# Performance work log

Hardware: AMD Instinct MI355X
Metric: run time of the kernel (lower is better)

Reference implementation:

```python
import jax, jax.numpy as jnp
import numpy as np

N = 10000   # nodes
E = 320000  # edges
G = 64      # graphs in batch
D = 256     # gnn embedding dim
A = 118     # atomic_num_dim
OUT = 100   # spectrum dim
NUM_GINE = 2


def setup_inputs() -> dict:
    key = jax.random.key(0)
    ks = jax.random.split(key, 16)
    inp = {
        'atomic_num': jax.random.normal(ks[0], (N, A), dtype=jnp.float32),
        'length': jax.random.uniform(ks[1], (E,), dtype=jnp.float32),
        'src': jax.random.randint(ks[2], (E,), 0, N, dtype=jnp.int32),
        'dst': jax.random.randint(ks[3], (E,), 0, N, dtype=jnp.int32),
        'graph_ids': jnp.sort(jax.random.randint(ks[4], (N,), 0, G, dtype=jnp.int32)),
        # parameters
        'W_node': jax.random.normal(ks[5], (A, D), dtype=jnp.float32) / np.sqrt(A),
        'b_node': jnp.zeros((D,), dtype=jnp.float32),
        'W_edge': jax.random.normal(ks[6], (1, D), dtype=jnp.float32),
        'b_edge': jnp.zeros((D,), dtype=jnp.float32),
        'gine_eps': jnp.zeros((NUM_GINE,), dtype=jnp.float32),  # learnable eps per GINEConv
        'W_gnn': jax.random.normal(ks[7], (NUM_GINE, D, D), dtype=jnp.float32) / np.sqrt(D),
        'b_gnn': jnp.zeros((NUM_GINE, D), dtype=jnp.float32),
        'eps_param': jnp.array([1e-3], dtype=jnp.float32),  # unify_vector eps
        'W_mlp': jax.random.normal(ks[8], (D, OUT), dtype=jnp.float32) / np.sqrt(D),
        'b_mlp': jnp.zeros((OUT,), dtype=jnp.float32),
    }
    return inp


def reference(atomic_num, length, src, dst, graph_ids,
              W_node, b_node, W_edge, b_edge,
              gine_eps, W_gnn, b_gnn, eps_param, W_mlp, b_mlp):
    # node / edge embeddings
    h = atomic_num @ W_node + b_node            # [N, D]
    e = length[:, None] @ W_edge + b_edge       # [E, D]
    # GINEConv layers: m_ij = relu(h_src + e_ij); h_i' = W((1+eps)h_i + sum_j m_ij) + b
    for i in range(NUM_GINE):
        m = jax.nn.relu(h[src] + e)             # [E, D] gather + elementwise
        agg = jax.ops.segment_sum(m, dst, num_segments=N)  # scatter-sum to dst nodes
        h = ((1.0 + gine_eps[i]) * h + agg) @ W_gnn[i] + b_gnn[i]
    # sum_nodes pooling per graph
    feat = jax.ops.segment_sum(h, graph_ids, num_segments=G)  # [G, D]
    # unify_vector: global min/max normalization
    mn = jnp.min(feat)
    mx = jnp.max(feat)
    feat = (feat - mn) / (eps_param[0] + mx - mn)
    # MLP head (no hidden layers): Linear(D, 100)
    return feat @ W_mlp + b_mlp                 # [G, 100]
```

## Files before the change

### kernel.cpp

```cpp
#include <hip/hip_runtime.h>
#include <hip/hip_bf16.h>

#define N_NODES 10000
#define N_EDGES 320000
#define N_GRAPHS 64
#define DIM 256
#define ADIM 118
#define OUTD 100
#define CAP 192

typedef short bf8_t __attribute__((ext_vector_type(8)));
typedef float f4_t  __attribute__((ext_vector_type(4)));

__device__ __forceinline__ unsigned short f2bf(float f) {
    unsigned u = __float_as_uint(f);
    u += 0x7FFFu + ((u >> 16) & 1u);
    return (unsigned short)(u >> 16);
}
__device__ __forceinline__ float bf2f(unsigned short s) {
    return __uint_as_float(((unsigned)s) << 16);
}

__global__ __launch_bounds__(256) void convW_k(
    const float* __restrict__ Wn, const float* __restrict__ Wg,
    unsigned short* __restrict__ WnT, unsigned short* __restrict__ WgT,
    int* __restrict__ cursor, float* __restrict__ feat) {
    int i = blockIdx.x * 256 + threadIdx.x;
    if (i < 32768) {
        int c = i >> 7, k = i & 127;
        WnT[i] = (k < ADIM) ? f2bf(Wn[k * DIM + c]) : (unsigned short)0;
    } else {
        int j = i - 32768;
        int l = j >> 16, rem = j & 65535;
        int c = rem >> 8, k = rem & 255;
        WgT[j] = f2bf(Wg[l * 65536 + k * DIM + c]);
    }
    if (i < N_NODES) cursor[i] = i * CAP;
    if (i < N_GRAPHS * DIM) feat[i] = 0.f;
}

__global__ __launch_bounds__(256) void fill_k(
    const int* __restrict__ src, const int* __restrict__ dst,
    const float* __restrict__ len, int* __restrict__ cursor,
    int2* __restrict__ epack) {
    int j = blockIdx.x * 256 + threadIdx.x;
    if (j >= N_EDGES) return;
    int d = dst[j];
    int pos = atomicAdd(&cursor[d], 1);
    if (pos < d * CAP + CAP)
        epack[pos] = make_int2(src[j], __float_as_int(len[j]));
}

#define AST 136
__global__ __launch_bounds__(256) void node_embed_k(
    const float* __restrict__ an, const unsigned short* __restrict__ WnT,
    const float* __restrict__ bn, unsigned short* __restrict__ hbf) {
    __shared__ unsigned short xs[16 * AST];
    const int base = blockIdx.x * 16;
    const int tid = threadIdx.x;
    for (int i = tid; i < 16 * (AST - ADIM); i += 256) {
        int r = i / (AST - ADIM);
        int c = i - r * (AST - ADIM);
        xs[r * AST + ADIM + c] = 0;
    }
    for (int i = tid; i < 16 * ADIM; i += 256) {
        int r = i / ADIM;
        int c = i - r * ADIM;
        xs[r * AST + c] = f2bf(an[(size_t)(base + r) * ADIM + c]);
    }
    __syncthreads();
    const int wave = tid >> 6, lane = tid & 63;
    const int m = lane & 15, quad = lane >> 4;
    bf8_t afrag[4];
    #pragma unroll
    for (int s = 0; s < 4; ++s)
        afrag[s] = *(const bf8_t*)&xs[m * AST + s * 32 + quad * 8];
    const int colbase = wave * 64;
    f4_t acc[4];
    #pragma unroll
    for (int ct = 0; ct < 4; ++ct) acc[ct] = (f4_t){0.f, 0.f, 0.f, 0.f};
    #pragma unroll
    for (int ct = 0; ct < 4; ++ct) {
        const unsigned short* wp = WnT + (size_t)(colbase + ct * 16 + m) * 128 + quad * 8;
        #pragma unroll
        for (int s = 0; s < 4; ++s) {
            bf8_t bfrag = *(const bf8_t*)(wp + s * 32);
            acc[ct] = __builtin_amdgcn_mfma_f32_16x16x32_bf16(afrag[s], bfrag, acc[ct], 0, 0, 0);
        }
    }
    #pragma unroll
    for (int ct = 0; ct < 4; ++ct) {
        int col = colbase + ct * 16 + m;
        float bb = bn[col];
        #pragma unroll
        for (int r = 0; r < 4; ++r)
            hbf[(size_t)(base + quad * 4 + r) * DIM + col] = f2bf(acc[ct][r] + bb);
    }
}

__global__ __launch_bounds__(256) void gather_k(
    const unsigned short* __restrict__ hbf, const int* __restrict__ cursor,
    const int2* __restrict__ epack, const float* __restrict__ We,
    const float* __restrict__ be, const float* __restrict__ epsp, int layer,
    unsigned short* __restrict__ xbf) {
    const int wave = threadIdx.x >> 6, lane = threadIdx.x & 63;
    const int node = __builtin_amdgcn_readfirstlane(blockIdx.x * 4 + wave);
    const int sub = lane >> 5;
    const int dp = (lane & 31) * 8;
    float4 wa = *(const float4*)(We + dp);
    float4 wc = *(const float4*)(We + dp + 4);
    float4 b0 = *(const float4*)(be + dp);
    float4 b1 = *(const float4*)(be + dp + 4);
    float w[8]  = {wa.x, wa.y, wa.z, wa.w, wc.x, wc.y, wc.z, wc.w};
    float bv[8] = {b0.x, b0.y, b0.z, b0.w, b1.x, b1.y, b1.z, b1.w};
    float acc[8];
    #pragma unroll
    for (int i = 0; i < 8; ++i) acc[i] = 0.f;
    const unsigned short* hb = hbf + dp;
    const int lo = node * CAP;
    const int cnt = min(__builtin_amdgcn_readfirstlane(cursor[node]) - lo, CAP);
    const int2* ep = epack + lo;
    int t = 0;
#define PAIR(pa, pb) { \
    int s = sub ? (pb).x : (pa).x; \
    float l = __int_as_float(sub ? (pb).y : (pa).y); \
    bf8_t a = *(const bf8_t*)(hb + (size_t)s * DIM); \
    _Pragma("unroll") \
    for (int d = 0; d < 8; ++d) \
        acc[d] += fmaxf(bf2f((unsigned short)a[d]) + fmaf(l, w[d], bv[d]), 0.f); }
    for (; t + 7 < cnt; t += 8) {
        int2 q0 = ep[t + 0], q1 = ep[t + 1], q2 = ep[t + 2], q3 = ep[t + 3];
        int2 q4 = ep[t + 4], q5 = ep[t + 5], q6 = ep[t + 6], q7 = ep[t + 7];
        PAIR(q0, q1) PAIR(q2, q3) PAIR(q4, q5) PAIR(q6, q7)
    }
    for (; t + 1 < cnt; t += 2) {
        int2 q0 = ep[t], q1 = ep[t + 1];
        PAIR(q0, q1)
    }
    if (t < cnt) {
        int2 q0 = ep[t];
        float l = __int_as_float(q0.y);
        bf8_t a = *(const bf8_t*)(hb + (size_t)q0.x * DIM);
        if (sub == 0) {
            #pragma unroll
            for (int d = 0; d < 8; ++d)
                acc[d] += fmaxf(bf2f((unsigned short)a[d]) + fmaf(l, w[d], bv[d]), 0.f);
        }
    }
#undef PAIR
    #pragma unroll
    for (int d = 0; d < 8; ++d)
        acc[d] += __shfl(acc[d], lane ^ 32, 64);
    if (sub == 0) {
        const float eps1 = 1.f + epsp[layer];
        bf8_t hv = *(const bf8_t*)(hbf + (size_t)node * DIM + dp);
        bf8_t o;
        #pragma unroll
        for (int d = 0; d < 8; ++d)
            o[d] = (short)f2bf(fmaf(eps1, bf2f((unsigned short)hv[d]), acc[d]));
        *(bf8_t*)(xbf + (size_t)node * DIM + dp) = o;
    }
}

#define XST 264
__global__ __launch_bounds__(256) void update_k(
    const unsigned short* __restrict__ xbf,
    const unsigned short* __restrict__ WT, const float* __restrict__ b,
    unsigned short* __restrict__ hout,
    const int* __restrict__ gid, float* __restrict__ feat, int do_pool) {
    __shared__ unsigned short xs[16 * XST];
    __shared__ int gids[16];
    const int rb = blockIdx.x >> 1;
    const int halfc = blockIdx.x & 1;
    const int base = rb * 16;
    const int tid = threadIdx.x;
    #pragma unroll
    for (int cch = tid; cch < 512; cch += 256) {
        int rr = cch >> 5, k0 = (cch & 31) * 8;
        *(bf8_t*)&xs[rr * XST + k0] = *(const bf8_t*)(xbf + (size_t)(base + rr) * DIM + k0);
    }
    if (do_pool && tid < 16) gids[tid] = gid[base + tid];
    __syncthreads();
    const int wave = tid >> 6, lane = tid & 63;
    const int m = lane & 15, quad = lane >> 4;
    bf8_t afrag[8];
    #pragma unroll
    for (int s = 0; s < 8; ++s)
        afrag[s] = *(const bf8_t*)&xs[m * XST + s * 32 + quad * 8];
    const int colbase = halfc * 128 + wave * 32;
    f4_t acc[2];
    #pragma unroll
    for (int ct = 0; ct < 2; ++ct) acc[ct] = (f4_t){0.f, 0.f, 0.f, 0.f};
    #pragma unroll
    for (int ct = 0; ct < 2; ++ct) {
        const unsigned short* wp = WT + (size_t)(colbase + ct * 16 + m) * DIM + quad * 8;
        #pragma unroll
        for (int s = 0; s < 8; ++s) {
            bf8_t bfrag = *(const bf8_t*)(wp + s * 32);
            acc[ct] = __builtin_amdgcn_mfma_f32_16x16x32_bf16(afrag[s], bfrag, acc[ct], 0, 0, 0);
        }
    }
    if (!do_pool) {
        #pragma unroll
        for (int ct = 0; ct < 2; ++ct) {
            int col = colbase + ct * 16 + m;
            float bb = b[col];
            #pragma unroll
            for (int r = 0; r < 4; ++r)
                hout[(size_t)(base + quad * 4 + r) * DIM + col] = f2bf(acc[ct][r] + bb);
        }
    } else {
        #pragma unroll
        for (int ct = 0; ct < 2; ++ct) {
            int col = colbase + ct * 16 + m;
            float bb = b[col];
            float run = 0.f;
            int cur = gids[quad * 4];
            #pragma unroll
            for (int r = 0; r < 4; ++r) {
                int g = gids[quad * 4 + r];
                if (g != cur) {
                    atomicAdd(&feat[(size_t)cur * DIM + col], run);
                    run = 0.f;
                    cur = g;
                }
                run += acc[ct][r] + bb;
            }
            atomicAdd(&feat[(size_t)cur * DIM + col], run);
        }
    }
}

__global__ __launch_bounds__(256) void headmm_k(
    const float* __restrict__ feat, const float* __restrict__ Wm,
    const float* __restrict__ bm, const float* __restrict__ epsp,
    float* __restrict__ out) {
    __shared__ float frow[DIM];
    __shared__ float smn[4], smx[4], sMn, sMx;
    const int g = blockIdx.x;
    const int tid = threadIdx.x;
    float mn = 3.4e38f, mx = -3.4e38f;
    for (int i = tid; i < N_GRAPHS * DIM; i += 256) {
        float v = feat[i];
        mn = fminf(mn, v);
        mx = fmaxf(mx, v);
    }
    frow[tid] = feat[g * DIM + tid];
    #pragma unroll
    for (int off = 32; off > 0; off >>= 1) {
        mn = fminf(mn, __shfl_down(mn, off, 64));
        mx = fmaxf(mx, __shfl_down(mx, off, 64));
    }
    const int wave = tid >> 6, lane = tid & 63;
    if (lane == 0) { smn[wave] = mn; smx[wave] = mx; }
    __syncthreads();
    if (tid == 0) {
        sMn = fminf(fminf(smn[0], smn[1]), fminf(smn[2], smn[3]));
        sMx = fmaxf(fmaxf(smx[0], smx[1]), fmaxf(smx[2], smx[3]));
    }
    __syncthreads();
    if (tid < OUTD) {
        const float mnv = sMn;
        const float inv = 1.f / (epsp[0] + sMx - mnv);
        float acc = 0.f;
        for (int d = 0; d < DIM; ++d)
            acc += (frow[d] - mnv) * Wm[d * OUTD + tid];
        out[g * OUTD + tid] = acc * inv + bm[tid];
    }
}

extern "C" void kernel_launch(void* const* d_in, const int* in_sizes, int n_in,
                              void* d_out, int out_size, void* d_ws, size_t ws_size,
                              hipStream_t stream) {
    const float* atomic_num = (const float*)d_in[0];
    const float* length     = (const float*)d_in[1];
    const int*   src        = (const int*)d_in[2];
    const int*   dst        = (const int*)d_in[3];
    const int*   gid        = (const int*)d_in[4];
    const float* W_node     = (const float*)d_in[5];
    const float* b_node     = (const float*)d_in[6];
    const float* W_edge     = (const float*)d_in[7];
    const float* b_edge     = (const float*)d_in[8];
    const float* gine_eps   = (const float*)d_in[9];
    const float* W_gnn      = (const float*)d_in[10];
    const float* b_gnn      = (const float*)d_in[11];
    const float* eps_param  = (const float*)d_in[12];
    const float* W_mlp      = (const float*)d_in[13];
    const float* b_mlp      = (const float*)d_in[14];
    float* out = (float*)d_out;

    float* feat = (float*)d_ws;
    int* cursor = (int*)(feat + (size_t)N_GRAPHS * DIM);
    int2* epack = (int2*)(cursor + N_NODES + 4);
    unsigned short* hbf0 = (unsigned short*)(epack + (size_t)N_NODES * CAP);
    unsigned short* hbf1 = hbf0 + (size_t)N_NODES * DIM;
    unsigned short* xbf  = hbf1 + (size_t)N_NODES * DIM;
    unsigned short* WnT  = xbf + (size_t)N_NODES * DIM;
    unsigned short* WgT  = WnT + 256 * 128;

    convW_k<<<640, 256, 0, stream>>>(W_node, W_gnn, WnT, WgT, cursor, feat);
    fill_k<<<N_EDGES / 256, 256, 0, stream>>>(src, dst, length, cursor, epack);
    node_embed_k<<<N_NODES / 16, 256, 0, stream>>>(atomic_num, WnT, b_node, hbf0);

    gather_k<<<N_NODES / 4, 256, 0, stream>>>(
        hbf0, cursor, epack, W_edge, b_edge, gine_eps, 0, xbf);
    update_k<<<(N_NODES / 16) * 2, 256, 0, stream>>>(
        xbf, WgT, b_gnn, hbf1, gid, feat, 0);
    gather_k<<<N_NODES / 4, 256, 0, stream>>>(
        hbf1, cursor, epack, W_edge, b_edge, gine_eps, 1, xbf);
    update_k<<<(N_NODES / 16) * 2, 256, 0, stream>>>(
        xbf, WgT + 256 * 256, b_gnn + DIM, hbf0, gid, feat, 1);

    headmm_k<<<N_GRAPHS, 256, 0, stream>>>(feat, W_mlp, b_mlp, eps_param, out);
}
```

Baseline: 216.9 us.

## Fuse neighbor gather with GINE linear update into one per-layer kernel

Merges the gather and update kernels into a single 1024-thread kernel. Each of its 16 waves aggregates one node's neighbors into shared memory, and the block then runs the 256x256 bf16 MFMA on the 16-row tile. This removes the intermediate xbf global round trip and two kernel launches per forward pass. Three smaller changes ride along: per-node atomic cursors are padded to 16 ints to reduce atomic contention in fill_k, node_embed loads use float2, and pooling adds a fast path that reduces with shuffles when all 16 rows share one graph. In exchange, each block now computes all 256 output columns with large blocks under a tighter register budget, and load imbalance across waves can stall the whole block at the barrier.

```diff
diff --git a/kernel.cpp b/kernel.cpp
--- a/kernel.cpp
+++ b/kernel.cpp
@@ -8,6 +8,7 @@
 #define ADIM 118
 #define OUTD 100
 #define CAP 192
+#define CURPAD 16
 
 typedef short bf8_t __attribute__((ext_vector_type(8)));
 typedef float f4_t  __attribute__((ext_vector_type(4)));
@@ -35,7 +36,7 @@
         int c = rem >> 8, k = rem & 255;
         WgT[j] = f2bf(Wg[l * 65536 + k * DIM + c]);
     }
-    if (i < N_NODES) cursor[i] = i * CAP;
+    if (i < N_NODES * CURPAD) cursor[i] = (i >> 4) * CAP;
     if (i < N_GRAPHS * DIM) feat[i] = 0.f;
 }
 
@@ -46,7 +47,7 @@
     int j = blockIdx.x * 256 + threadIdx.x;
     if (j >= N_EDGES) return;
     int d = dst[j];
-    int pos = atomicAdd(&cursor[d], 1);
+    int pos = atomicAdd(&cursor[d << 4], 1);
     if (pos < d * CAP + CAP)
         epack[pos] = make_int2(src[j], __float_as_int(len[j]));
 }
@@ -55,7 +56,7 @@
 __global__ __launch_bounds__(256) void node_embed_k(
     const float* __restrict__ an, const unsigned short* __restrict__ WnT,
     const float* __restrict__ bn, unsigned short* __restrict__ hbf) {
-    __shared__ unsigned short xs[16 * AST];
+    __shared__ __attribute__((aligned(16))) unsigned short xs[16 * AST];
     const int base = blockIdx.x * 16;
     const int tid = threadIdx.x;
     for (int i = tid; i < 16 * (AST - ADIM); i += 256) {
@@ -63,10 +64,12 @@
         int c = i - r * (AST - ADIM);
         xs[r * AST + ADIM + c] = 0;
     }
-    for (int i = tid; i < 16 * ADIM; i += 256) {
-        int r = i / ADIM;
-        int c = i - r * ADIM;
-        xs[r * AST + c] = f2bf(an[(size_t)(base + r) * ADIM + c]);
+    for (int i = tid; i < 16 * 59; i += 256) {
+        int r = i / 59;
+        int c = (i - r * 59) * 2;
+        float2 v = *(const float2*)(an + (size_t)(base + r) * ADIM + c);
+        xs[r * AST + c]     = f2bf(v.x);
+        xs[r * AST + c + 1] = f2bf(v.y);
     }
     __syncthreads();
     const int wave = tid >> 6, lane = tid & 63;
@@ -98,13 +101,21 @@
     }
 }
 
-__global__ __launch_bounds__(256) void gather_k(
+#define XST 264
+__global__ __launch_bounds__(1024, 4) void layer_k(
     const unsigned short* __restrict__ hbf, const int* __restrict__ cursor,
     const int2* __restrict__ epack, const float* __restrict__ We,
     const float* __restrict__ be, const float* __restrict__ epsp, int layer,
-    unsigned short* __restrict__ xbf) {
-    const int wave = threadIdx.x >> 6, lane = threadIdx.x & 63;
-    const int node = __builtin_amdgcn_readfirstlane(blockIdx.x * 4 + wave);
+    const unsigned short* __restrict__ WT, const float* __restrict__ bvec,
+    unsigned short* __restrict__ hout, const int* __restrict__ gid,
+    float* __restrict__ feat, int do_pool) {
+    __shared__ __attribute__((aligned(16))) unsigned short xs[16 * XST];
+    __shared__ int gids[16];
+    const int tid = threadIdx.x;
+    const int wave = tid >> 6, lane = tid & 63;
+    const int base = blockIdx.x * 16;
+
+    const int node = __builtin_amdgcn_readfirstlane(base + wave);
     const int sub = lane >> 5;
     const int dp = (lane & 31) * 8;
     float4 wa = *(const float4*)(We + dp);
@@ -118,7 +129,7 @@
     for (int i = 0; i < 8; ++i) acc[i] = 0.f;
     const unsigned short* hb = hbf + dp;
     const int lo = node * CAP;
-    const int cnt = min(__builtin_amdgcn_readfirstlane(cursor[node]) - lo, CAP);
+    const int cnt = min(__builtin_amdgcn_readfirstlane(cursor[node * CURPAD]) - lo, CAP);
     const int2* ep = epack + lo;
     int t = 0;
 #define PAIR(pa, pb) { \
@@ -158,62 +169,36 @@
         #pragma unroll
         for (int d = 0; d < 8; ++d)
             o[d] = (short)f2bf(fmaf(eps1, bf2f((unsigned short)hv[d]), acc[d]));
-        *(bf8_t*)(xbf + (size_t)node * DIM + dp) = o;
-    }
-}
-
-#define XST 264
-__global__ __launch_bounds__(256) void update_k(
-    const unsigned short* __restrict__ xbf,
-    const unsigned short* __restrict__ WT, const float* __restrict__ b,
-    unsigned short* __restrict__ hout,
-    const int* __restrict__ gid, float* __restrict__ feat, int do_pool) {
-    __shared__ unsigned short xs[16 * XST];
-    __shared__ int gids[16];
-    const int rb = blockIdx.x >> 1;
-    const int halfc = blockIdx.x & 1;
-    const int base = rb * 16;
-    const int tid = threadIdx.x;
-    #pragma unroll
-    for (int cch = tid; cch < 512; cch += 256) {
-        int rr = cch >> 5, k0 = (cch & 31) * 8;
-        *(bf8_t*)&xs[rr * XST + k0] = *(const bf8_t*)(xbf + (size_t)(base + rr) * DIM + k0);
+        *(bf8_t*)&xs[wave * XST + dp] = o;
     }
     if (do_pool && tid < 16) gids[tid] = gid[base + tid];
     __syncthreads();
-    const int wave = tid >> 6, lane = tid & 63;
+
     const int m = lane & 15, quad = lane >> 4;
     bf8_t afrag[8];
     #pragma unroll
     for (int s = 0; s < 8; ++s)
         afrag[s] = *(const bf8_t*)&xs[m * XST + s * 32 + quad * 8];
-    const int colbase = halfc * 128 + wave * 32;
-    f4_t acc[2];
-    #pragma unroll
-    for (int ct = 0; ct < 2; ++ct) acc[ct] = (f4_t){0.f, 0.f, 0.f, 0.f};
-    #pragma unroll
-    for (int ct = 0; ct < 2; ++ct) {
-        const unsigned short* wp = WT + (size_t)(colbase + ct * 16 + m) * DIM + quad * 8;
-        #pragma unroll
-        for (int s = 0; s < 8; ++s) {
-            bf8_t bfrag = *(const bf8_t*)(wp + s * 32);
-            acc[ct] = __builtin_amdgcn_mfma_f32_16x16x32_bf16(afrag[s], bfrag, acc[ct], 0, 0, 0);
-        }
-    }
+    const int col = wave * 16 + m;
+    f4_t acc2 = (f4_t){0.f, 0.f, 0.f, 0.f};
+    const unsigned short* wp = WT + (size_t)col * DIM + quad * 8;
+    #pragma unroll
+    for (int s = 0; s < 8; ++s) {
+        bf8_t bfrag = *(const bf8_t*)(wp + s * 32);
+        acc2 = __builtin_amdgcn_mfma_f32_16x16x32_bf16(afrag[s], bfrag, acc2, 0, 0, 0);
+    }
+    const float bb = bvec[col];
     if (!do_pool) {
         #pragma unroll
-        for (int ct = 0; ct < 2; ++ct) {
-            int col = colbase + ct * 16 + m;
-            float bb = b[col];
-            #pragma unroll
-            for (int r = 0; r < 4; ++r)
-                hout[(size_t)(base + quad * 4 + r) * DIM + col] = f2bf(acc[ct][r] + bb);
-        }
+        for (int r = 0; r < 4; ++r)
+            hout[(size_t)(base + quad * 4 + r) * DIM + col] = f2bf(acc2[r] + bb);
     } else {
-        #pragma unroll
-        for (int ct = 0; ct < 2; ++ct) {
-            int col = colbase + ct * 16 + m;
-            float bb = b[col];
+        if (gids[0] == gids[15]) {
+            float v = acc2[0] + acc2[1] + acc2[2] + acc2[3] + 4.f * bb;
+            v += __shfl(v, lane ^ 16, 64);
+            v += __shfl(v, lane ^ 32, 64);
+            if (quad == 0) atomicAdd(&feat[(size_t)gids[0] * DIM + col], v);
+        } else {
             float run = 0.f;
             int cur = gids[quad * 4];
             #pragma unroll
@@ -224,7 +209,7 @@
                     run = 0.f;
                     cur = g;
                 }
-                run += acc[ct][r] + bb;
+                run += acc2[r] + bb;
             }
             atomicAdd(&feat[(size_t)cur * DIM + col], run);
         }
@@ -291,25 +276,22 @@
 
     float* feat = (float*)d_ws;
     int* cursor = (int*)(feat + (size_t)N_GRAPHS * DIM);
-    int2* epack = (int2*)(cursor + N_NODES + 4);
+    int2* epack = (int2*)(cursor + (size_t)N_NODES * CURPAD + 16);
     unsigned short* hbf0 = (unsigned short*)(epack + (size_t)N_NODES * CAP);
     unsigned short* hbf1 = hbf0 + (size_t)N_NODES * DIM;
-    unsigned short* xbf  = hbf1 + (size_t)N_NODES * DIM;
-    unsigned short* WnT  = xbf + (size_t)N_NODES * DIM;
+    unsigned short* WnT  = hbf1 + (size_t)N_NODES * DIM;
     unsigned short* WgT  = WnT + 256 * 128;
 
     convW_k<<<640, 256, 0, stream>>>(W_node, W_gnn, WnT, WgT, cursor, feat);
     fill_k<<<N_EDGES / 256, 256, 0, stream>>>(src, dst, length, cursor, epack);
     node_embed_k<<<N_NODES / 16, 256, 0, stream>>>(atomic_num, WnT, b_node, hbf0);
 
-    gather_k<<<N_NODES / 4, 256, 0, stream>>>(
-        hbf0, cursor, epack, W_edge, b_edge, gine_eps, 0, xbf);
-    update_k<<<(N_NODES / 16) * 2, 256, 0, stream>>>(
-        xbf, WgT, b_gnn, hbf1, gid, feat, 0);
-    gather_k<<<N_NODES / 4, 256, 0, stream>>>(
-        hbf1, cursor, epack, W_edge, b_edge, gine_eps, 1, xbf);
-    update_k<<<(N_NODES / 16) * 2, 256, 0, stream>>>(
-        xbf, WgT + 256 * 256, b_gnn + DIM, hbf0, gid, feat, 1);
+    layer_k<<<N_NODES / 16, 1024, 0, stream>>>(
+        hbf0, cursor, epack, W_edge, b_edge, gine_eps, 0,
+        WgT, b_gnn, hbf1, gid, feat, 0);
+    layer_k<<<N_NODES / 16, 1024, 0, stream>>>(
+        hbf1, cursor, epack, W_edge, b_edge, gine_eps, 1,
+        WgT + 256 * 256, b_gnn + DIM, hbf0, gid, feat, 1);
 
     headmm_k<<<N_GRAPHS, 256, 0, stream>>>(feat, W_mlp, b_mlp, eps_param, out);
 }
```

New measurement: 211.5 us. 2.5% less time.
